# Optimization experiments

Hardware: AMD Instinct MI355X
Metric: run time of the kernel (lower is better)

The kernel has to match this reference:

```python
import jax, jax.numpy as jnp
import numpy as np

B, C, H, W = 4, 3, 128, 128
HID = 128          # hidden_features
L = 6              # hidden_layers
NP = 5             # n_params
DT = 0.1
EPS = 1e-5         # PyG InstanceNorm eps
D_EMB = 1 + 2 + NP             # u + pos(2) + params
D_MSG = 2 * HID + 1 + 2 + NP   # x_i,x_j,u_i-u_j,pos_i-pos_j,vars_i
D_UPD = HID + HID + NP         # x, message, vars


def _build_edges(b, h, w):
    # 8-neighbor grid graph (radius_graph with r=sqrt(2), loop=False),
    # node index = ix*h + iy (x-major, matching create_graph's meshgrid flatten)
    ix, iy = np.meshgrid(np.arange(w), np.arange(h), indexing='ij')
    node = ix * h + iy
    srcs, tgts = [], []
    for dx in (-1, 0, 1):
        for dy in (-1, 0, 1):
            if dx == 0 and dy == 0:
                continue
            t = node[max(0, -dx):w - max(0, dx), max(0, -dy):h - max(0, dy)]
            s = node[max(0, dx):w - max(0, -dx), max(0, dy):h - max(0, -dy)]
            srcs.append(s.ravel()); tgts.append(t.ravel())
    src = np.concatenate(srcs); tgt = np.concatenate(tgts)
    offs = (np.arange(b) * h * w)[:, None]
    src = (src[None, :] + offs).ravel()
    tgt = (tgt[None, :] + offs).ravel()
    return np.stack([src, tgt]).astype(np.int32)


def _lin(key, fan_in, fan_out):
    kw, kb = jax.random.split(key)
    s = 1.0 / np.sqrt(fan_in)
    return (jax.random.uniform(kw, (fan_in, fan_out), jnp.float32, -s, s),
            jax.random.uniform(kb, (fan_out,), jnp.float32, -s, s))


def setup_inputs() -> dict:
    key = jax.random.key(0)
    ks = jax.random.split(key, 32)
    inputs = jax.random.normal(ks[0], (B, C, H, W), jnp.float32)
    case_params = jax.random.uniform(ks[1], (B, NP), jnp.float32, 0.5, 1.5)
    edge_index = jnp.asarray(_build_edges(B, H, W))

    emb_W1, emb_b1 = _lin(ks[2], D_EMB, HID)
    emb_W2, emb_b2 = _lin(ks[3], HID, HID)

    def stack(kbase, fan_in, fan_out):
        Ws, bs = [], []
        for l in range(L):
            Wl, bl = _lin(jax.random.fold_in(kbase, l), fan_in, fan_out)
            Ws.append(Wl); bs.append(bl)
        return jnp.stack(Ws), jnp.stack(bs)

    msg1_W, msg1_b = stack(ks[4], D_MSG, HID)
    msg2_W, msg2_b = stack(ks[5], HID, HID)
    upd1_W, upd1_b = stack(ks[6], D_UPD, HID)
    upd2_W, upd2_b = stack(ks[7], HID, HID)
    out_W1, out_b1 = _lin(ks[8], HID, HID // 2)
    out_W2, out_b2 = _lin(ks[9], HID // 2, 1)

    return dict(inputs=inputs, case_params=case_params, edge_index=edge_index,
                emb_W1=emb_W1, emb_b1=emb_b1, emb_W2=emb_W2, emb_b2=emb_b2,
                msg1_W=msg1_W, msg1_b=msg1_b, msg2_W=msg2_W, msg2_b=msg2_b,
                upd1_W=upd1_W, upd1_b=upd1_b, upd2_W=upd2_W, upd2_b=upd2_b,
                out_W1=out_W1, out_b1=out_b1, out_W2=out_W2, out_b2=out_b2)


def reference(inputs, case_params, edge_index,
              emb_W1, emb_b1, emb_W2, emb_b2,
              msg1_W, msg1_b, msg2_W, msg2_b,
              upd1_W, upd1_b, upd2_W, upd2_b,
              out_W1, out_b1, out_W2, out_b2):
    b, c, h, w = inputs.shape
    n = b * h * w
    swish = lambda x: x * jax.nn.sigmoid(x)

    # graph node features: [b,c,h,w] -> [b*h*w, c]; u = channel 0
    x_nodes = inputs.transpose(0, 2, 3, 1).reshape(-1, c)
    u = x_nodes[:, :1]
    # pos, faithful to create_graph: per-graph meshgrid over (x:w, y:h), x-major flatten
    gx = jnp.linspace(0., 1., w)[:, None] * jnp.ones((h,), inputs.dtype)   # [w,h]
    gy = jnp.ones((w,), inputs.dtype)[:, None] * jnp.linspace(0., 1., h)  # [w,h]
    pos = jnp.stack([gx[None] * case_params[:, 1, None, None],
                     gy[None] * case_params[:, 0, None, None]], axis=-1).reshape(-1, 2)
    params = jnp.repeat(case_params, h * w, axis=0)  # [n, NP]

    src, tgt = edge_index[0], edge_index[1]
    deg = jax.ops.segment_sum(jnp.ones_like(src, dtype=inputs.dtype), tgt,
                              num_segments=n)
    deg = jnp.maximum(deg, 1.)[:, None]

    # embedding MLP
    f = swish(jnp.concatenate([u, pos, params], -1) @ emb_W1 + emb_b1)
    f = swish(f @ emb_W2 + emb_b2)

    for l in range(msg1_W.shape[0]):
        # message: gather -> MLP (formula 8)
        m = jnp.concatenate([f[tgt], f[src], u[tgt] - u[src],
                             pos[tgt] - pos[src], params[tgt]], -1)  # [E, D_MSG]
        m = swish(m @ msg1_W[l] + msg1_b[l])
        m = swish(m @ msg2_W[l] + msg2_b[l])
        # mean-aggregate at target nodes
        agg = jax.ops.segment_sum(m, tgt, num_segments=n) / deg
        # update MLP (formula 9) + residual (in_features == out_features)
        upd = swish(jnp.concatenate([f, agg, params], -1) @ upd1_W[l] + upd1_b[l])
        upd = swish(upd @ upd2_W[l] + upd2_b[l])
        f = f + upd
        # InstanceNorm per graph (affine=False, biased var)
        fg = f.reshape(b, h * w, -1)
        mean = fg.mean(1, keepdims=True)
        var = ((fg - mean) ** 2).mean(1, keepdims=True)
        f = ((fg - mean) * jax.lax.rsqrt(var + EPS)).reshape(n, -1)

    diff = swish(f @ out_W1 + out_b1) @ out_W2 + out_b2  # [n,1]
    out = u + DT * diff
    return out.reshape(b, h, w, 1).transpose(0, 3, 1, 2)  # preds [b,1,h,w]
```

## Files before the change

kernel.cpp:

```cpp
#include <hip/hip_runtime.h>
#include <hip/hip_bf16.h>
#include <math.h>

#define NNODE 65536
#define NBAT  16384
#define NP    5
#define DT    0.1f
#define EPS   1e-5f

typedef __attribute__((ext_vector_type(8))) short short8;
typedef __attribute__((ext_vector_type(4))) float floatx4;

union S8U { short8 s; unsigned int u[4]; };

__device__ __forceinline__ float swishf(float x) {
    return x * __builtin_amdgcn_rcpf(1.f + __expf(-x));
}
__device__ __forceinline__ float asf(unsigned int u) {
    union { unsigned int u; float f; } x; x.u = u; return x.f;
}
__device__ __forceinline__ unsigned short f2b(float f) {
    union { float f; unsigned int u; } x; x.f = f;
    unsigned int r = x.u + 0x7fff + ((x.u >> 16) & 1);
    return (unsigned short)(r >> 16);
}
__device__ __forceinline__ unsigned int pk2(float a, float b) {
    __hip_bfloat162 h = __float22bfloat162_rn(make_float2(a, b));
    union { __hip_bfloat162 h; unsigned int u; } x; x.h = h; return x.u;
}

#define CHP(w, g, r15) ((((w) * 272) + (g) * 17 + (r15)) * 8)

__global__ __launch_bounds__(256) void prep_frag(
    const float* __restrict__ src, unsigned short* __restrict__ dst,
    int ldn, int koff, int NT, int lstride, int perm, int total)
{
    int i = blockIdx.x * 256 + threadIdx.x;
    if (i >= total) return;
    int nper = NT << 11;
    int l = i / nper;
    int r0 = i - l * nper;
    int t = r0 >> 11;
    int ks = (r0 >> 9) & 3;
    int lane = (r0 >> 3) & 63;
    int j = r0 & 7;
    int lm = lane & 15, lq = lane >> 4;
    int p = ks * 32 + lq * 8 + j;
    int k = perm ? ((p & 7) * 16 + (p >> 3)) : p;
    int n = t * 16 + lm;
    dst[i] = f2b(src[(size_t)l * lstride + (size_t)(koff + k) * ldn + n]);
}

__global__ __launch_bounds__(256) void node_init(
    const float* __restrict__ inp, const float* __restrict__ cp,
    float* __restrict__ u, float* __restrict__ posx, float* __restrict__ posy,
    float* __restrict__ mr)
{
    int n = blockIdx.x * 256 + threadIdx.x;
    int b = n >> 14, r = n & 16383;
    int a = r >> 7, c = r & 127;
    u[n] = inp[b * 3 * NBAT + r];
    posx[n] = (a * (1.f / 127.f)) * cp[b * NP + 1];
    posy[n] = (c * (1.f / 127.f)) * cp[b * NP + 0];
    if (n < 1024) mr[n] = ((n >> 7) & 1) ? 1.f : 0.f;
}

__device__ __forceinline__ void build_normf_frags(
    const float* __restrict__ f, const float* __restrict__ mr,
    int block0, int b, int w, int lm, int lq, short8* afr)
{
    int row = block0 + w * 16 + lm;
#pragma unroll
    for (int ks = 0; ks < 4; ks++) {
        int po = ks * 32 + lq * 8;
        float4 v0 = *(const float4*)(f + (size_t)row * 128 + po);
        float4 v1 = *(const float4*)(f + (size_t)row * 128 + po + 4);
        float4 m0 = *(const float4*)(mr + b * 256 + po);
        float4 m1 = *(const float4*)(mr + b * 256 + po + 4);
        float4 s0 = *(const float4*)(mr + b * 256 + 128 + po);
        float4 s1 = *(const float4*)(mr + b * 256 + 128 + po + 4);
        S8U o;
        o.u[0] = pk2((v0.x - m0.x) * s0.x, (v0.y - m0.y) * s0.y);
        o.u[1] = pk2((v0.z - m0.z) * s0.z, (v0.w - m0.w) * s0.w);
        o.u[2] = pk2((v1.x - m1.x) * s1.x, (v1.y - m1.y) * s1.y);
        o.u[3] = pk2((v1.z - m1.z) * s1.z, (v1.w - m1.w) * s1.w);
        afr[ks] = o.s;
    }
}

__global__ __launch_bounds__(256) void embed_mfma(
    const float* __restrict__ u, const float* __restrict__ posx,
    const float* __restrict__ posy, const float* __restrict__ cp,
    const float* __restrict__ W1, const float* __restrict__ b1,
    const unsigned short* __restrict__ W2F, const float* __restrict__ b2,
    float* __restrict__ f)
{
    __shared__ unsigned short lA[4 * 272 * 8];
    __shared__ unsigned short lB[1024 * 8];
    int tid = threadIdx.x;
    int block0 = blockIdx.x * 64;
    {
        int r = tid >> 2, p4 = tid & 3;
        int n = block0 + r;
        int b = n >> 14;
        float e8[8];
        e8[0] = u[n]; e8[1] = posx[n]; e8[2] = posy[n];
#pragma unroll
        for (int p = 0; p < 5; p++) e8[3 + p] = cp[b * NP + p];
        float a32[32];
        const float4* b4 = (const float4*)(b1 + p4 * 32);
#pragma unroll
        for (int q = 0; q < 8; q++) {
            float4 bv = b4[q];
            a32[q * 4 + 0] = bv.x; a32[q * 4 + 1] = bv.y;
            a32[q * 4 + 2] = bv.z; a32[q * 4 + 3] = bv.w;
        }
#pragma unroll
        for (int i = 0; i < 8; i++) {
            const float4* w4 = (const float4*)(W1 + i * 128 + p4 * 32);
            float ev = e8[i];
#pragma unroll
            for (int q = 0; q < 8; q++) {
                float4 wv = w4[q];
                a32[q * 4 + 0] += ev * wv.x; a32[q * 4 + 1] += ev * wv.y;
                a32[q * 4 + 2] += ev * wv.z; a32[q * 4 + 3] += ev * wv.w;
            }
        }
#pragma unroll
        for (int j = 0; j < 4; j++) {
            S8U o;
#pragma unroll
            for (int q = 0; q < 4; q++)
                o.u[q] = pk2(swishf(a32[j * 8 + 2 * q]), swishf(a32[j * 8 + 2 * q + 1]));
            *(short8*)(lA + CHP(r >> 4, p4 * 4 + j, r & 15)) = o.s;
        }
    }
    int w = tid >> 6, lane = tid & 63, lm = lane & 15, lq = lane >> 4;
    floatx4 acc[8];
#pragma unroll
    for (int t = 0; t < 8; t++) acc[t] = (floatx4)(0.f);
    for (int th = 0; th < 2; th++) {
        if (th) __syncthreads();
#pragma unroll
        for (int i = 0; i < 4; i++)
            *(short8*)(lB + (tid + i * 256) * 8) =
                *(const short8*)(W2F + (th * 1024 + tid + i * 256) * 8);
        __syncthreads();
#pragma unroll
        for (int ks = 0; ks < 4; ks++) {
            short8 a = *(const short8*)(lA + CHP(w, ks * 4 + lq, lm));
#pragma unroll
            for (int t2 = 0; t2 < 4; t2++) {
                short8 bf = *(const short8*)(lB + ((t2 * 4 + ks) * 64 + lane) * 8);
                acc[th * 4 + t2] = __builtin_amdgcn_mfma_f32_16x16x32_bf16(a, bf, acc[th * 4 + t2], 0, 0, 0);
            }
        }
    }
    float bias2[8];
#pragma unroll
    for (int t = 0; t < 8; t++) bias2[t] = b2[t * 16 + lm];
#pragma unroll
    for (int r = 0; r < 4; r++) {
        int nd = block0 + w * 16 + lq * 4 + r;
        float4 v0, v1;
        v0.x = swishf(acc[0][r] + bias2[0]); v0.y = swishf(acc[1][r] + bias2[1]);
        v0.z = swishf(acc[2][r] + bias2[2]); v0.w = swishf(acc[3][r] + bias2[3]);
        v1.x = swishf(acc[4][r] + bias2[4]); v1.y = swishf(acc[5][r] + bias2[5]);
        v1.z = swishf(acc[6][r] + bias2[6]); v1.w = swishf(acc[7][r] + bias2[7]);
        *(float4*)(f + (size_t)nd * 128 + lm * 8) = v0;
        *(float4*)(f + (size_t)nd * 128 + lm * 8 + 4) = v1;
    }
}

__global__ __launch_bounds__(256) void pqu_kernel(
    const float* __restrict__ f, const float* __restrict__ mr,
    const unsigned short* __restrict__ wPT, const unsigned short* __restrict__ wQT,
    const float* __restrict__ mW, const float* __restrict__ mb,
    const float* __restrict__ u, const float* __restrict__ px,
    const float* __restrict__ py, const float* __restrict__ cp,
    unsigned short* __restrict__ Pn, unsigned short* __restrict__ Qn)
{
    __shared__ unsigned short lB[2048 * 8];
    int tid = threadIdx.x;
    int block0 = blockIdx.x * 64;
    int b = block0 >> 14;
    int w = tid >> 6, lane = tid & 63, lm = lane & 15, lq = lane >> 4;

    short8 afr[4];
    build_normf_frags(f, mr, block0, b, w, lm, lq, afr);

    float u4[4], px4[4], py4[4];
#pragma unroll
    for (int r = 0; r < 4; r++) {
        int nd = block0 + w * 16 + lq * 4 + r;
        u4[r] = u[nd]; px4[r] = px[nd]; py4[r] = py[nd];
    }
    float cp5[5];
#pragma unroll
    for (int p = 0; p < 5; p++) cp5[p] = cp[b * NP + p];
    float wu[8], wx[8], wy[8], pt[8];

    for (int ph = 0; ph < 2; ph++) {
        const unsigned short* bsrc = (ph == 0) ? wPT : wQT;
        if (ph) __syncthreads();
#pragma unroll
        for (int i = 0; i < 8; i++)
            *(short8*)(lB + (tid + i * 256) * 8) = *(const short8*)(bsrc + (tid + i * 256) * 8);
        __syncthreads();
        floatx4 acc[8];
#pragma unroll
        for (int t = 0; t < 8; t++) acc[t] = (floatx4)(0.f);
#pragma unroll
        for (int ks = 0; ks < 4; ks++) {
#pragma unroll
            for (int t = 0; t < 8; t++) {
                short8 bf = *(const short8*)(lB + ((t * 4 + ks) * 64 + lane) * 8);
                acc[t] = __builtin_amdgcn_mfma_f32_16x16x32_bf16(afr[ks], bf, acc[t], 0, 0, 0);
            }
        }
        if (ph == 0) {
#pragma unroll
            for (int t = 0; t < 8; t++) {
                int c = t * 16 + lm;
                wu[t] = mW[256 * 128 + c]; wx[t] = mW[257 * 128 + c]; wy[t] = mW[258 * 128 + c];
                float p0 = mb[c];
#pragma unroll
                for (int p = 0; p < 5; p++) p0 += cp5[p] * mW[(259 + p) * 128 + c];
                pt[t] = p0;
            }
#pragma unroll
            for (int r = 0; r < 4; r++) {
                int nd = block0 + w * 16 + lq * 4 + r;
                float v[8];
#pragma unroll
                for (int t = 0; t < 8; t++)
                    v[t] = acc[t][r] + pt[t] + u4[r] * wu[t] + px4[r] * wx[t] + py4[r] * wy[t];
                S8U o;
#pragma unroll
                for (int q = 0; q < 4; q++) o.u[q] = pk2(v[2 * q], v[2 * q + 1]);
                *(short8*)(Pn + (size_t)nd * 128 + lm * 8) = o.s;
            }
        } else {
#pragma unroll
            for (int r = 0; r < 4; r++) {
                int nd = block0 + w * 16 + lq * 4 + r;
                float v[8];
#pragma unroll
                for (int t = 0; t < 8; t++)
                    v[t] = acc[t][r] - (u4[r] * wu[t] + px4[r] * wx[t] + py4[r] * wy[t]);
                S8U o;
#pragma unroll
                for (int q = 0; q < 4; q++) o.u[q] = pk2(v[2 * q], v[2 * q + 1]);
                *(short8*)(Qn + (size_t)nd * 128 + lm * 8) = o.s;
            }
        }
    }
}

__global__ __launch_bounds__(256) void msg_kernel(
    const unsigned short* __restrict__ Pn, const unsigned short* __restrict__ Qn,
    const unsigned short* __restrict__ w2F, const float* __restrict__ b2,
    unsigned short* __restrict__ aggF)
{
    __shared__ unsigned short lB[1024 * 8];
    __shared__ unsigned short lAgg[8 * 128];
    int tid = threadIdx.x;
    int base = blockIdx.x * 8;
    int b = base >> 14;
    int a = (base >> 7) & 127;
    int c0 = base & 127;
    int w = tid >> 6, lane = tid & 63, lm = lane & 15, lq = lane >> 4;

    short8 afr[4];
    {
        int tl = lm >> 3, e = lm & 7;
        int idx = (e < 4) ? e : e + 1;
        int dx = idx / 3 - 1, dy = idx % 3 - 1;
        int cc = c0 + w * 2 + tl;
        int na = a + dx, nc = cc + dy;
        bool valid = (na >= 0) & (na < 128) & (nc >= 0) & (nc < 128);
        int t = base + w * 2 + tl;
        int s = valid ? ((b << 14) + (na << 7) + nc) : t;
#pragma unroll
        for (int ks = 0; ks < 4; ks++) {
            int po = ks * 32 + lq * 8;
            S8U pv, qv, o;
            pv.s = *(const short8*)(Pn + (size_t)t * 128 + po);
            qv.s = *(const short8*)(Qn + (size_t)s * 128 + po);
#pragma unroll
            for (int q = 0; q < 4; q++) {
                float pl = asf(pv.u[q] << 16), ph = asf(pv.u[q] & 0xffff0000u);
                float ql = asf(qv.u[q] << 16), qh = asf(qv.u[q] & 0xffff0000u);
                o.u[q] = pk2(swishf(pl + ql), swishf(ph + qh));
            }
            afr[ks] = o.s;
        }
    }

    floatx4 acc[8];
#pragma unroll
    for (int t = 0; t < 8; t++) acc[t] = (floatx4)(0.f);
    for (int th = 0; th < 2; th++) {
        if (th) __syncthreads();
#pragma unroll
        for (int i = 0; i < 4; i++)
            *(short8*)(lB + (tid + i * 256) * 8) =
                *(const short8*)(w2F + (th * 1024 + tid + i * 256) * 8);
        __syncthreads();
#pragma unroll
        for (int ks = 0; ks < 4; ks++) {
#pragma unroll
            for (int t2 = 0; t2 < 4; t2++) {
                short8 bf = *(const short8*)(lB + ((t2 * 4 + ks) * 64 + lane) * 8);
                acc[th * 4 + t2] = __builtin_amdgcn_mfma_f32_16x16x32_bf16(afr[ks], bf, acc[th * 4 + t2], 0, 0, 0);
            }
        }
    }

    bool vr[4];
#pragma unroll
    for (int r = 0; r < 4; r++) {
        int row16 = lq * 4 + r;
        int tl2 = row16 >> 3, e = row16 & 7;
        int idx = (e < 4) ? e : e + 1;
        int dx = idx / 3 - 1, dy = idx % 3 - 1;
        int cc = c0 + w * 2 + tl2;
        int na = a + dx, nc = cc + dy;
        vr[r] = (na >= 0) & (na < 128) & (nc >= 0) & (nc < 128);
    }
    float ov[8];
#pragma unroll
    for (int t = 0; t < 8; t++) {
        float bb = b2[t * 16 + lm];
        float s01 = 0.f;
#pragma unroll
        for (int r = 0; r < 4; r++)
            s01 += vr[r] ? swishf(acc[t][r] + bb) : 0.f;
        ov[t] = s01 + __shfl_xor(s01, 16);
    }
    if ((lq & 1) == 0) {
        int tl = w * 2 + (lq >> 1);
        int cc = c0 + tl;
        int deg = (1 + (a > 0) + (a < 127)) * (1 + (cc > 0) + (cc < 127)) - 1;
        float inv = 1.f / (float)deg;
        S8U o;
#pragma unroll
        for (int q = 0; q < 4; q++) o.u[q] = pk2(ov[2 * q] * inv, ov[2 * q + 1] * inv);
        *(short8*)(lAgg + tl * 128 + lm * 8) = o.s;
    }
    __syncthreads();
    if (tid < 128) {
        int row8 = tid >> 4, g = tid & 15;
        int n = base + row8;
        size_t lin = (size_t)(n >> 6) * 1024 + (size_t)(((n & 63) >> 4) * 256 + g * 16 + (n & 15));
        *(short8*)(aggF + lin * 8) = *(const short8*)(lAgg + row8 * 128 + g * 8);
    }
}

__global__ __launch_bounds__(256) void updf_kernel(
    float* __restrict__ f, const float* __restrict__ mr,
    const unsigned short* __restrict__ aggF,
    const unsigned short* __restrict__ u1aF, const unsigned short* __restrict__ u1bF,
    const unsigned short* __restrict__ u2F,
    const float* __restrict__ U1, const float* __restrict__ c1,
    const float* __restrict__ c2, const float* __restrict__ cp,
    float* __restrict__ partials)
{
    __shared__ unsigned short lA[4 * 272 * 8];
    __shared__ unsigned short lB[1024 * 8];
    int tid = threadIdx.x;
    int block0 = blockIdx.x * 64;
    int b = block0 >> 14;
    int w = tid >> 6, lane = tid & 63, lm = lane & 15, lq = lane >> 4;

    short8 afr[4];
    build_normf_frags(f, mr, block0, b, w, lm, lq, afr);
    floatx4 acc[8];
#pragma unroll
    for (int t = 0; t < 8; t++) acc[t] = (floatx4)(0.f);

    for (int ph = 0; ph < 2; ph++) {
        const unsigned short* bsrc = ph ? u1bF : u1aF;
        if (ph) {
#pragma unroll
            for (int ks = 0; ks < 4; ks++)
                afr[ks] = *(const short8*)(aggF +
                    ((size_t)blockIdx.x * 1024 + w * 256 + (ks * 4 + lq) * 16 + lm) * 8);
        }
        for (int th = 0; th < 2; th++) {
            if (ph | th) __syncthreads();
#pragma unroll
            for (int i = 0; i < 4; i++)
                *(short8*)(lB + (tid + i * 256) * 8) =
                    *(const short8*)(bsrc + (th * 1024 + tid + i * 256) * 8);
            __syncthreads();
#pragma unroll
            for (int ks = 0; ks < 4; ks++) {
#pragma unroll
                for (int t2 = 0; t2 < 4; t2++) {
                    short8 bf = *(const short8*)(lB + ((t2 * 4 + ks) * 64 + lane) * 8);
                    acc[th * 4 + t2] = __builtin_amdgcn_mfma_f32_16x16x32_bf16(afr[ks], bf, acc[th * 4 + t2], 0, 0, 0);
                }
            }
        }
    }

    float cp5[5];
#pragma unroll
    for (int p = 0; p < 5; p++) cp5[p] = cp[b * NP + p];
    float pt[8];
#pragma unroll
    for (int t = 0; t < 8; t++) {
        int c = t * 16 + lm;
        float p0 = c1[c];
#pragma unroll
        for (int p = 0; p < 5; p++) p0 += cp5[p] * U1[(256 + p) * 128 + c];
        pt[t] = p0;
    }
#pragma unroll
    for (int r = 0; r < 4; r++) {
        S8U o;
#pragma unroll
        for (int q = 0; q < 4; q++)
            o.u[q] = pk2(swishf(acc[2 * q][r] + pt[2 * q]),
                         swishf(acc[2 * q + 1][r] + pt[2 * q + 1]));
        *(short8*)(lA + CHP(w, lm, lq * 4 + r)) = o.s;
    }

#pragma unroll
    for (int t = 0; t < 8; t++) acc[t] = (floatx4)(0.f);
    for (int th = 0; th < 2; th++) {
        __syncthreads();
#pragma unroll
        for (int i = 0; i < 4; i++)
            *(short8*)(lB + (tid + i * 256) * 8) =
                *(const short8*)(u2F + (th * 1024 + tid + i * 256) * 8);
        __syncthreads();
#pragma unroll
        for (int ks = 0; ks < 4; ks++) {
            short8 a = *(const short8*)(lA + CHP(w, ks * 4 + lq, lm));
#pragma unroll
            for (int t2 = 0; t2 < 4; t2++) {
                short8 bf = *(const short8*)(lB + ((t2 * 4 + ks) * 64 + lane) * 8);
                acc[th * 4 + t2] = __builtin_amdgcn_mfma_f32_16x16x32_bf16(a, bf, acc[th * 4 + t2], 0, 0, 0);
            }
        }
    }

    float c2v[8];
#pragma unroll
    for (int t = 0; t < 8; t++) c2v[t] = c2[t * 16 + lm];
    float4 me0 = *(const float4*)(mr + b * 256 + lm * 8);
    float4 me1 = *(const float4*)(mr + b * 256 + lm * 8 + 4);
    float4 rs0 = *(const float4*)(mr + b * 256 + 128 + lm * 8);
    float4 rs1 = *(const float4*)(mr + b * 256 + 128 + lm * 8 + 4);
    float ssum[8], ssq[8];
#pragma unroll
    for (int t = 0; t < 8; t++) { ssum[t] = 0.f; ssq[t] = 0.f; }
#pragma unroll
    for (int r = 0; r < 4; r++) {
        int nd = block0 + w * 16 + lq * 4 + r;
        float4 f0 = *(const float4*)(f + (size_t)nd * 128 + lm * 8);
        float4 f1 = *(const float4*)(f + (size_t)nd * 128 + lm * 8 + 4);
        float fn[8];
        fn[0] = (f0.x - me0.x) * rs0.x + swishf(acc[0][r] + c2v[0]);
        fn[1] = (f0.y - me0.y) * rs0.y + swishf(acc[1][r] + c2v[1]);
        fn[2] = (f0.z - me0.z) * rs0.z + swishf(acc[2][r] + c2v[2]);
        fn[3] = (f0.w - me0.w) * rs0.w + swishf(acc[3][r] + c2v[3]);
        fn[4] = (f1.x - me1.x) * rs1.x + swishf(acc[4][r] + c2v[4]);
        fn[5] = (f1.y - me1.y) * rs1.y + swishf(acc[5][r] + c2v[5]);
        fn[6] = (f1.z - me1.z) * rs1.z + swishf(acc[6][r] + c2v[6]);
        fn[7] = (f1.w - me1.w) * rs1.w + swishf(acc[7][r] + c2v[7]);
        *(float4*)(f + (size_t)nd * 128 + lm * 8) = make_float4(fn[0], fn[1], fn[2], fn[3]);
        *(float4*)(f + (size_t)nd * 128 + lm * 8 + 4) = make_float4(fn[4], fn[5], fn[6], fn[7]);
#pragma unroll
        for (int t = 0; t < 8; t++) { ssum[t] += fn[t]; ssq[t] += fn[t] * fn[t]; }
    }
#pragma unroll
    for (int t = 0; t < 8; t++) {
        ssum[t] += __shfl_xor(ssum[t], 16); ssum[t] += __shfl_xor(ssum[t], 32);
        ssq[t]  += __shfl_xor(ssq[t], 16);  ssq[t]  += __shfl_xor(ssq[t], 32);
    }
    __syncthreads();
    float* red = (float*)lA;
    if (lq == 0) {
#pragma unroll
        for (int t = 0; t < 8; t++) {
            red[w * 256 + lm * 8 + t] = ssum[t];
            red[w * 256 + 128 + lm * 8 + t] = ssq[t];
        }
    }
    __syncthreads();
    {
        float v = red[tid] + red[256 + tid] + red[512 + tid] + red[768 + tid];
        partials[(size_t)blockIdx.x * 256 + tid] = v;
    }
}

__global__ __launch_bounds__(256) void finalize_kernel(
    const float* __restrict__ partials, float* __restrict__ mr)
{
    __shared__ float s[256];
    int b = blockIdx.x, tid = threadIdx.x;
    float acc = 0.f;
    const float* p = partials + (size_t)b * 256 * 256 + tid;
#pragma unroll 8
    for (int i = 0; i < 256; i++) acc += p[i * 256];
    s[tid] = acc;
    __syncthreads();
    if (tid < 128) {
        float mean = s[tid] * (1.f / 16384.f);
        float var = s[128 + tid] * (1.f / 16384.f) - mean * mean;
        mr[b * 256 + tid] = mean;
        mr[b * 256 + 128 + tid] = rsqrtf(var + EPS);
    }
}

__global__ __launch_bounds__(256) void out_head(
    const float* __restrict__ f, const float* __restrict__ mr,
    const unsigned short* __restrict__ O1F, const float* __restrict__ ob1,
    const float* __restrict__ O2, const float* __restrict__ ob2,
    const float* __restrict__ u, float* __restrict__ out)
{
    __shared__ unsigned short lB[1024 * 8];
    int tid = threadIdx.x;
    int block0 = blockIdx.x * 64;
    int b = block0 >> 14;
    int w = tid >> 6, lane = tid & 63, lm = lane & 15, lq = lane >> 4;
#pragma unroll
    for (int i = 0; i < 4; i++)
        *(short8*)(lB + (tid + i * 256) * 8) = *(const short8*)(O1F + (tid + i * 256) * 8);
    short8 afr[4];
    build_normf_frags(f, mr, block0, b, w, lm, lq, afr);
    __syncthreads();
    floatx4 acc[4];
#pragma unroll
    for (int t = 0; t < 4; t++) acc[t] = (floatx4)(0.f);
#pragma unroll
    for (int ks = 0; ks < 4; ks++) {
#pragma unroll
        for (int t = 0; t < 4; t++) {
            short8 bf = *(const short8*)(lB + ((t * 4 + ks) * 64 + lane) * 8);
            acc[t] = __builtin_amdgcn_mfma_f32_16x16x32_bf16(afr[ks], bf, acc[t], 0, 0, 0);
        }
    }
    float b1v[4], o2v[4];
#pragma unroll
    for (int t = 0; t < 4; t++) {
        b1v[t] = ob1[t * 16 + lm];
        o2v[t] = O2[t * 16 + lm];
    }
    float ob2v = ob2[0];
#pragma unroll
    for (int r = 0; r < 4; r++) {
        float s = 0.f;
#pragma unroll
        for (int t = 0; t < 4; t++) s += swishf(acc[t][r] + b1v[t]) * o2v[t];
        s += __shfl_xor(s, 1); s += __shfl_xor(s, 2);
        s += __shfl_xor(s, 4); s += __shfl_xor(s, 8);
        if (lm == 0) {
            int nd = block0 + w * 16 + lq * 4 + r;
            out[nd] = u[nd] + DT * (s + ob2v);
        }
    }
}

extern "C" void kernel_launch(void* const* d_in, const int* in_sizes, int n_in,
                              void* d_out, int out_size, void* d_ws, size_t ws_size,
                              hipStream_t stream)
{
    const float* inputs = (const float*)d_in[0];
    const float* cp     = (const float*)d_in[1];
    const float* emb_W1 = (const float*)d_in[3];
    const float* emb_b1 = (const float*)d_in[4];
    const float* emb_W2 = (const float*)d_in[5];
    const float* emb_b2 = (const float*)d_in[6];
    const float* msg1_W = (const float*)d_in[7];
    const float* msg1_b = (const float*)d_in[8];
    const float* msg2_W = (const float*)d_in[9];
    const float* msg2_b = (const float*)d_in[10];
    const float* upd1_W = (const float*)d_in[11];
    const float* upd1_b = (const float*)d_in[12];
    const float* upd2_W = (const float*)d_in[13];
    const float* upd2_b = (const float*)d_in[14];
    const float* out_W1 = (const float*)d_in[15];
    const float* out_b1 = (const float*)d_in[16];
    const float* out_W2 = (const float*)d_in[17];
    const float* out_b2 = (const float*)d_in[18];
    float* out = (float*)d_out;

    char* base = (char*)d_ws;
    size_t off = 0;
    float* f     = (float*)(base + off); off += (size_t)NNODE * 128 * 4;
    unsigned short* Pn   = (unsigned short*)(base + off); off += (size_t)NNODE * 128 * 2;
    unsigned short* Qn   = (unsigned short*)(base + off); off += (size_t)NNODE * 128 * 2;
    unsigned short* aggF = (unsigned short*)(base + off); off += (size_t)NNODE * 128 * 2;
    float* u    = (float*)(base + off); off += NNODE * 4;
    float* posx = (float*)(base + off); off += NNODE * 4;
    float* posy = (float*)(base + off); off += NNODE * 4;
    float* partials = (float*)(base + off); off += 1024 * 256 * 4;
    float* mrbuf = (float*)(base + off); off += 1024 * 4;
    unsigned short* wPT  = (unsigned short*)(base + off); off += 6 * 16384 * 2;
    unsigned short* wQT  = (unsigned short*)(base + off); off += 6 * 16384 * 2;
    unsigned short* w2F  = (unsigned short*)(base + off); off += 6 * 16384 * 2;
    unsigned short* u1aF = (unsigned short*)(base + off); off += 6 * 16384 * 2;
    unsigned short* u1bF = (unsigned short*)(base + off); off += 6 * 16384 * 2;
    unsigned short* u2F  = (unsigned short*)(base + off); off += 6 * 16384 * 2;
    unsigned short* eW2F = (unsigned short*)(base + off); off += 16384 * 2;
    unsigned short* O1F  = (unsigned short*)(base + off); off += 8192 * 2;

    prep_frag<<<384, 256, 0, stream>>>(msg1_W, wPT, 128, 0,   8, 264 * 128, 1, 6 * 16384);
    prep_frag<<<384, 256, 0, stream>>>(msg1_W, wQT, 128, 128, 8, 264 * 128, 1, 6 * 16384);
    prep_frag<<<384, 256, 0, stream>>>(msg2_W, w2F, 128, 0,   8, 128 * 128, 1, 6 * 16384);
    prep_frag<<<384, 256, 0, stream>>>(upd1_W, u1aF, 128, 0,   8, 261 * 128, 1, 6 * 16384);
    prep_frag<<<384, 256, 0, stream>>>(upd1_W, u1bF, 128, 128, 8, 261 * 128, 1, 6 * 16384);
    prep_frag<<<384, 256, 0, stream>>>(upd2_W, u2F, 128, 0,   8, 128 * 128, 1, 6 * 16384);
    prep_frag<<<64, 256, 0, stream>>>(emb_W2, eW2F, 128, 0,   8, 0, 0, 16384);
    prep_frag<<<32, 256, 0, stream>>>(out_W1, O1F, 64, 0,    4, 0, 1, 8192);

    node_init<<<256, 256, 0, stream>>>(inputs, cp, u, posx, posy, mrbuf);
    embed_mfma<<<1024, 256, 0, stream>>>(u, posx, posy, cp, emb_W1, emb_b1, eW2F, emb_b2, f);
    for (int l = 0; l < 6; l++) {
        pqu_kernel<<<1024, 256, 0, stream>>>(f, mrbuf,
            wPT + (size_t)l * 16384, wQT + (size_t)l * 16384,
            msg1_W + (size_t)l * 264 * 128, msg1_b + (size_t)l * 128,
            u, posx, posy, cp, Pn, Qn);
        msg_kernel<<<8192, 256, 0, stream>>>(Pn, Qn,
            w2F + (size_t)l * 16384, msg2_b + (size_t)l * 128, aggF);
        updf_kernel<<<1024, 256, 0, stream>>>(f, mrbuf, aggF,
            u1aF + (size_t)l * 16384, u1bF + (size_t)l * 16384, u2F + (size_t)l * 16384,
            upd1_W + (size_t)l * 261 * 128, upd1_b + (size_t)l * 128,
            upd2_b + (size_t)l * 128, cp, partials);
        finalize_kernel<<<4, 256, 0, stream>>>(partials, mrbuf);
    }
    out_head<<<1024, 256, 0, stream>>>(f, mrbuf, O1F, out_b1, out_W2, out_b2, u, out);
}
```

Baseline: 801.1 us.

## Merge prep launches, fuse node init into embed, store P/Q in fp32, fold biases

Eight weight-prep launches become one prep_all kernel, and node_init is folded into embed_mfma, removing several small launches. The P/Q message intermediates are now stored as fp32 rather than bf16. This doubles their memory traffic in the gather-heavy msg_kernel but drops the unpack step and gains precision. Biases are preloaded into the MFMA accumulators across kernels. msg_kernel also gets a fast path for interior tiles that skips neighbour-validity checks and uses a constant degree of 8.

After: 852.6 us. 6.4% more time.

```diff
diff --git a/kernel.cpp b/kernel.cpp
--- a/kernel.cpp
+++ b/kernel.cpp
@@ -16,9 +16,6 @@
 __device__ __forceinline__ float swishf(float x) {
     return x * __builtin_amdgcn_rcpf(1.f + __expf(-x));
 }
-__device__ __forceinline__ float asf(unsigned int u) {
-    union { unsigned int u; float f; } x; x.u = u; return x.f;
-}
 __device__ __forceinline__ unsigned short f2b(float f) {
     union { float f; unsigned int u; } x; x.f = f;
     unsigned int r = x.u + 0x7fff + ((x.u >> 16) & 1);
@@ -31,12 +28,27 @@
 
 #define CHP(w, g, r15) ((((w) * 272) + (g) * 17 + (r15)) * 8)
 
-__global__ __launch_bounds__(256) void prep_frag(
-    const float* __restrict__ src, unsigned short* __restrict__ dst,
-    int ldn, int koff, int NT, int lstride, int perm, int total)
-{
-    int i = blockIdx.x * 256 + threadIdx.x;
-    if (i >= total) return;
+__global__ __launch_bounds__(256) void prep_all(
+    const float* __restrict__ msg1_W, const float* __restrict__ msg2_W,
+    const float* __restrict__ upd1_W, const float* __restrict__ upd2_W,
+    const float* __restrict__ emb_W2, const float* __restrict__ out_W1,
+    unsigned short* __restrict__ wPT, unsigned short* __restrict__ wQT,
+    unsigned short* __restrict__ w2F, unsigned short* __restrict__ u1aF,
+    unsigned short* __restrict__ u1bF, unsigned short* __restrict__ u2F,
+    unsigned short* __restrict__ eW2F, unsigned short* __restrict__ O1F)
+{
+    int blk = blockIdx.x;
+    const float* src; unsigned short* dst;
+    int ldn = 128, koff, NT = 8, lstride, perm = 1, i0;
+    if (blk < 384)       { src = msg1_W; dst = wPT;  koff = 0;   lstride = 264 * 128; i0 = blk; }
+    else if (blk < 768)  { src = msg1_W; dst = wQT;  koff = 128; lstride = 264 * 128; i0 = blk - 384; }
+    else if (blk < 1152) { src = msg2_W; dst = w2F;  koff = 0;   lstride = 128 * 128; i0 = blk - 768; }
+    else if (blk < 1536) { src = upd1_W; dst = u1aF; koff = 0;   lstride = 261 * 128; i0 = blk - 1152; }
+    else if (blk < 1920) { src = upd1_W; dst = u1bF; koff = 128; lstride = 261 * 128; i0 = blk - 1536; }
+    else if (blk < 2304) { src = upd2_W; dst = u2F;  koff = 0;   lstride = 128 * 128; i0 = blk - 1920; }
+    else if (blk < 2368) { src = emb_W2; dst = eW2F; koff = 0;   lstride = 0; perm = 0; i0 = blk - 2304; }
+    else                 { src = out_W1; dst = O1F;  koff = 0;   lstride = 0; ldn = 64; NT = 4; i0 = blk - 2368; }
+    int i = i0 * 256 + threadIdx.x;
     int nper = NT << 11;
     int l = i / nper;
     int r0 = i - l * nper;
@@ -49,20 +61,6 @@
     int k = perm ? ((p & 7) * 16 + (p >> 3)) : p;
     int n = t * 16 + lm;
     dst[i] = f2b(src[(size_t)l * lstride + (size_t)(koff + k) * ldn + n]);
-}
-
-__global__ __launch_bounds__(256) void node_init(
-    const float* __restrict__ inp, const float* __restrict__ cp,
-    float* __restrict__ u, float* __restrict__ posx, float* __restrict__ posy,
-    float* __restrict__ mr)
-{
-    int n = blockIdx.x * 256 + threadIdx.x;
-    int b = n >> 14, r = n & 16383;
-    int a = r >> 7, c = r & 127;
-    u[n] = inp[b * 3 * NBAT + r];
-    posx[n] = (a * (1.f / 127.f)) * cp[b * NP + 1];
-    posy[n] = (c * (1.f / 127.f)) * cp[b * NP + 0];
-    if (n < 1024) mr[n] = ((n >> 7) & 1) ? 1.f : 0.f;
 }
 
 __device__ __forceinline__ void build_normf_frags(
@@ -89,22 +87,29 @@
 }
 
 __global__ __launch_bounds__(256) void embed_mfma(
-    const float* __restrict__ u, const float* __restrict__ posx,
-    const float* __restrict__ posy, const float* __restrict__ cp,
+    const float* __restrict__ inp, const float* __restrict__ cp,
     const float* __restrict__ W1, const float* __restrict__ b1,
     const unsigned short* __restrict__ W2F, const float* __restrict__ b2,
-    float* __restrict__ f)
+    float* __restrict__ f, float* __restrict__ u,
+    float* __restrict__ posx, float* __restrict__ posy, float* __restrict__ mr)
 {
     __shared__ unsigned short lA[4 * 272 * 8];
     __shared__ unsigned short lB[1024 * 8];
     int tid = threadIdx.x;
     int block0 = blockIdx.x * 64;
+    if (blockIdx.x < 4) mr[blockIdx.x * 256 + tid] = ((tid >> 7) & 1) ? 1.f : 0.f;
     {
         int r = tid >> 2, p4 = tid & 3;
         int n = block0 + r;
         int b = n >> 14;
+        int rr = n & 16383;
+        int aa = rr >> 7, cc = rr & 127;
+        float uu = inp[b * 3 * NBAT + rr];
+        float pxx = (aa * (1.f / 127.f)) * cp[b * NP + 1];
+        float pyy = (cc * (1.f / 127.f)) * cp[b * NP + 0];
+        if (p4 == 0) { u[n] = uu; posx[n] = pxx; posy[n] = pyy; }
         float e8[8];
-        e8[0] = u[n]; e8[1] = posx[n]; e8[2] = posy[n];
+        e8[0] = uu; e8[1] = pxx; e8[2] = pyy;
 #pragma unroll
         for (int p = 0; p < 5; p++) e8[3 + p] = cp[b * NP + p];
         float a32[32];
@@ -136,9 +141,12 @@
         }
     }
     int w = tid >> 6, lane = tid & 63, lm = lane & 15, lq = lane >> 4;
+    float bias2[8];
+#pragma unroll
+    for (int t = 0; t < 8; t++) bias2[t] = b2[t * 16 + lm];
     floatx4 acc[8];
 #pragma unroll
-    for (int t = 0; t < 8; t++) acc[t] = (floatx4)(0.f);
+    for (int t = 0; t < 8; t++) acc[t] = (floatx4)(bias2[t]);
     for (int th = 0; th < 2; th++) {
         if (th) __syncthreads();
 #pragma unroll
@@ -156,17 +164,14 @@
             }
         }
     }
-    float bias2[8];
-#pragma unroll
-    for (int t = 0; t < 8; t++) bias2[t] = b2[t * 16 + lm];
 #pragma unroll
     for (int r = 0; r < 4; r++) {
         int nd = block0 + w * 16 + lq * 4 + r;
         float4 v0, v1;
-        v0.x = swishf(acc[0][r] + bias2[0]); v0.y = swishf(acc[1][r] + bias2[1]);
-        v0.z = swishf(acc[2][r] + bias2[2]); v0.w = swishf(acc[3][r] + bias2[3]);
-        v1.x = swishf(acc[4][r] + bias2[4]); v1.y = swishf(acc[5][r] + bias2[5]);
-        v1.z = swishf(acc[6][r] + bias2[6]); v1.w = swishf(acc[7][r] + bias2[7]);
+        v0.x = swishf(acc[0][r]); v0.y = swishf(acc[1][r]);
+        v0.z = swishf(acc[2][r]); v0.w = swishf(acc[3][r]);
+        v1.x = swishf(acc[4][r]); v1.y = swishf(acc[5][r]);
+        v1.z = swishf(acc[6][r]); v1.w = swishf(acc[7][r]);
         *(float4*)(f + (size_t)nd * 128 + lm * 8) = v0;
         *(float4*)(f + (size_t)nd * 128 + lm * 8 + 4) = v1;
     }
@@ -178,7 +183,7 @@
     const float* __restrict__ mW, const float* __restrict__ mb,
     const float* __restrict__ u, const float* __restrict__ px,
     const float* __restrict__ py, const float* __restrict__ cp,
-    unsigned short* __restrict__ Pn, unsigned short* __restrict__ Qn)
+    float* __restrict__ Pn, float* __restrict__ Qn)
 {
     __shared__ unsigned short lB[2048 * 8];
     int tid = threadIdx.x;
@@ -199,6 +204,15 @@
 #pragma unroll
     for (int p = 0; p < 5; p++) cp5[p] = cp[b * NP + p];
     float wu[8], wx[8], wy[8], pt[8];
+#pragma unroll
+    for (int t = 0; t < 8; t++) {
+        int c = t * 16 + lm;
+        wu[t] = mW[256 * 128 + c]; wx[t] = mW[257 * 128 + c]; wy[t] = mW[258 * 128 + c];
+        float p0 = mb[c];
+#pragma unroll
+        for (int p = 0; p < 5; p++) p0 += cp5[p] * mW[(259 + p) * 128 + c];
+        pt[t] = p0;
+    }
 
     for (int ph = 0; ph < 2; ph++) {
         const unsigned short* bsrc = (ph == 0) ? wPT : wQT;
@@ -209,7 +223,7 @@
         __syncthreads();
         floatx4 acc[8];
 #pragma unroll
-        for (int t = 0; t < 8; t++) acc[t] = (floatx4)(0.f);
+        for (int t = 0; t < 8; t++) acc[t] = (ph == 0) ? (floatx4)(pt[t]) : (floatx4)(0.f);
 #pragma unroll
         for (int ks = 0; ks < 4; ks++) {
 #pragma unroll
@@ -220,45 +234,44 @@
         }
         if (ph == 0) {
 #pragma unroll
-            for (int t = 0; t < 8; t++) {
-                int c = t * 16 + lm;
-                wu[t] = mW[256 * 128 + c]; wx[t] = mW[257 * 128 + c]; wy[t] = mW[258 * 128 + c];
-                float p0 = mb[c];
-#pragma unroll
-                for (int p = 0; p < 5; p++) p0 += cp5[p] * mW[(259 + p) * 128 + c];
-                pt[t] = p0;
-            }
-#pragma unroll
             for (int r = 0; r < 4; r++) {
                 int nd = block0 + w * 16 + lq * 4 + r;
-                float v[8];
-#pragma unroll
-                for (int t = 0; t < 8; t++)
-                    v[t] = acc[t][r] + pt[t] + u4[r] * wu[t] + px4[r] * wx[t] + py4[r] * wy[t];
-                S8U o;
-#pragma unroll
-                for (int q = 0; q < 4; q++) o.u[q] = pk2(v[2 * q], v[2 * q + 1]);
-                *(short8*)(Pn + (size_t)nd * 128 + lm * 8) = o.s;
+                float sc0 = u4[r], sc1 = px4[r], sc2 = py4[r];
+                float4 o0, o1;
+                o0.x = acc[0][r] + sc0 * wu[0] + sc1 * wx[0] + sc2 * wy[0];
+                o0.y = acc[1][r] + sc0 * wu[1] + sc1 * wx[1] + sc2 * wy[1];
+                o0.z = acc[2][r] + sc0 * wu[2] + sc1 * wx[2] + sc2 * wy[2];
+                o0.w = acc[3][r] + sc0 * wu[3] + sc1 * wx[3] + sc2 * wy[3];
+                o1.x = acc[4][r] + sc0 * wu[4] + sc1 * wx[4] + sc2 * wy[4];
+                o1.y = acc[5][r] + sc0 * wu[5] + sc1 * wx[5] + sc2 * wy[5];
+                o1.z = acc[6][r] + sc0 * wu[6] + sc1 * wx[6] + sc2 * wy[6];
+                o1.w = acc[7][r] + sc0 * wu[7] + sc1 * wx[7] + sc2 * wy[7];
+                *(float4*)(Pn + (size_t)nd * 128 + lm * 8) = o0;
+                *(float4*)(Pn + (size_t)nd * 128 + lm * 8 + 4) = o1;
             }
         } else {
 #pragma unroll
             for (int r = 0; r < 4; r++) {
                 int nd = block0 + w * 16 + lq * 4 + r;
-                float v[8];
-#pragma unroll
-                for (int t = 0; t < 8; t++)
-                    v[t] = acc[t][r] - (u4[r] * wu[t] + px4[r] * wx[t] + py4[r] * wy[t]);
-                S8U o;
-#pragma unroll
-                for (int q = 0; q < 4; q++) o.u[q] = pk2(v[2 * q], v[2 * q + 1]);
-                *(short8*)(Qn + (size_t)nd * 128 + lm * 8) = o.s;
+                float sc0 = u4[r], sc1 = px4[r], sc2 = py4[r];
+                float4 o0, o1;
+                o0.x = acc[0][r] - (sc0 * wu[0] + sc1 * wx[0] + sc2 * wy[0]);
+                o0.y = acc[1][r] - (sc0 * wu[1] + sc1 * wx[1] + sc2 * wy[1]);
+                o0.z = acc[2][r] - (sc0 * wu[2] + sc1 * wx[2] + sc2 * wy[2]);
+                o0.w = acc[3][r] - (sc0 * wu[3] + sc1 * wx[3] + sc2 * wy[3]);
+                o1.x = acc[4][r] - (sc0 * wu[4] + sc1 * wx[4] + sc2 * wy[4]);
+                o1.y = acc[5][r] - (sc0 * wu[5] + sc1 * wx[5] + sc2 * wy[5]);
+                o1.z = acc[6][r] - (sc0 * wu[6] + sc1 * wx[6] + sc2 * wy[6]);
+                o1.w = acc[7][r] - (sc0 * wu[7] + sc1 * wx[7] + sc2 * wy[7]);
+                *(float4*)(Qn + (size_t)nd * 128 + lm * 8) = o0;
+                *(float4*)(Qn + (size_t)nd * 128 + lm * 8 + 4) = o1;
             }
         }
     }
 }
 
 __global__ __launch_bounds__(256) void msg_kernel(
-    const unsigned short* __restrict__ Pn, const unsigned short* __restrict__ Qn,
+    const float* __restrict__ Pn, const float* __restrict__ Qn,
     const unsigned short* __restrict__ w2F, const float* __restrict__ b2,
     unsigned short* __restrict__ aggF)
 {
@@ -270,6 +283,7 @@
     int a = (base >> 7) & 127;
     int c0 = base & 127;
     int w = tid >> 6, lane = tid & 63, lm = lane & 15, lq = lane >> 4;
+    bool interior = (a > 0) & (a < 127) & (c0 > 0) & (c0 + 8 < 128);
 
     short8 afr[4];
     {
@@ -278,28 +292,37 @@
         int dx = idx / 3 - 1, dy = idx % 3 - 1;
         int cc = c0 + w * 2 + tl;
         int na = a + dx, nc = cc + dy;
-        bool valid = (na >= 0) & (na < 128) & (nc >= 0) & (nc < 128);
         int t = base + w * 2 + tl;
-        int s = valid ? ((b << 14) + (na << 7) + nc) : t;
+        int s;
+        if (interior) s = (b << 14) + (na << 7) + nc;
+        else {
+            bool valid = (na >= 0) & (na < 128) & (nc >= 0) & (nc < 128);
+            s = valid ? ((b << 14) + (na << 7) + nc) : t;
+        }
+        const float* Pr = Pn + (size_t)t * 128;
+        const float* Qr = Qn + (size_t)s * 128;
 #pragma unroll
         for (int ks = 0; ks < 4; ks++) {
             int po = ks * 32 + lq * 8;
-            S8U pv, qv, o;
-            pv.s = *(const short8*)(Pn + (size_t)t * 128 + po);
-            qv.s = *(const short8*)(Qn + (size_t)s * 128 + po);
-#pragma unroll
-            for (int q = 0; q < 4; q++) {
-                float pl = asf(pv.u[q] << 16), ph = asf(pv.u[q] & 0xffff0000u);
-                float ql = asf(qv.u[q] << 16), qh = asf(qv.u[q] & 0xffff0000u);
-                o.u[q] = pk2(swishf(pl + ql), swishf(ph + qh));
-            }
+            float4 p0 = *(const float4*)(Pr + po);
+            float4 p1 = *(const float4*)(Pr + po + 4);
+            float4 q0 = *(const float4*)(Qr + po);
+            float4 q1 = *(const float4*)(Qr + po + 4);
+            S8U o;
+            o.u[0] = pk2(swishf(p0.x + q0.x), swishf(p0.y + q0.y));
+            o.u[1] = pk2(swishf(p0.z + q0.z), swishf(p0.w + q0.w));
+            o.u[2] = pk2(swishf(p1.x + q1.x), swishf(p1.y + q1.y));
+            o.u[3] = pk2(swishf(p1.z + q1.z), swishf(p1.w + q1.w));
             afr[ks] = o.s;
         }
     }
 
+    float b2v[8];
+#pragma unroll
+    for (int t = 0; t < 8; t++) b2v[t] = b2[t * 16 + lm];
     floatx4 acc[8];
 #pragma unroll
-    for (int t = 0; t < 8; t++) acc[t] = (floatx4)(0.f);
+    for (int t = 0; t < 8; t++) acc[t] = (floatx4)(b2v[t]);
     for (int th = 0; th < 2; th++) {
         if (th) __syncthreads();
 #pragma unroll
@@ -317,36 +340,53 @@
         }
     }
 
-    bool vr[4];
-#pragma unroll
-    for (int r = 0; r < 4; r++) {
-        int row16 = lq * 4 + r;
-        int tl2 = row16 >> 3, e = row16 & 7;
-        int idx = (e < 4) ? e : e + 1;
-        int dx = idx / 3 - 1, dy = idx % 3 - 1;
-        int cc = c0 + w * 2 + tl2;
-        int na = a + dx, nc = cc + dy;
-        vr[r] = (na >= 0) & (na < 128) & (nc >= 0) & (nc < 128);
-    }
-    float ov[8];
-#pragma unroll
-    for (int t = 0; t < 8; t++) {
-        float bb = b2[t * 16 + lm];
-        float s01 = 0.f;
-#pragma unroll
-        for (int r = 0; r < 4; r++)
-            s01 += vr[r] ? swishf(acc[t][r] + bb) : 0.f;
-        ov[t] = s01 + __shfl_xor(s01, 16);
-    }
-    if ((lq & 1) == 0) {
-        int tl = w * 2 + (lq >> 1);
-        int cc = c0 + tl;
-        int deg = (1 + (a > 0) + (a < 127)) * (1 + (cc > 0) + (cc < 127)) - 1;
-        float inv = 1.f / (float)deg;
-        S8U o;
-#pragma unroll
-        for (int q = 0; q < 4; q++) o.u[q] = pk2(ov[2 * q] * inv, ov[2 * q + 1] * inv);
-        *(short8*)(lAgg + tl * 128 + lm * 8) = o.s;
+    if (interior) {
+        float ov[8];
+#pragma unroll
+        for (int t = 0; t < 8; t++) {
+            float s01 = swishf(acc[t][0]) + swishf(acc[t][1])
+                      + swishf(acc[t][2]) + swishf(acc[t][3]);
+            ov[t] = s01 + __shfl_xor(s01, 16);
+        }
+        if ((lq & 1) == 0) {
+            int tl = w * 2 + (lq >> 1);
+            S8U o;
+#pragma unroll
+            for (int q = 0; q < 4; q++)
+                o.u[q] = pk2(ov[2 * q] * 0.125f, ov[2 * q + 1] * 0.125f);
+            *(short8*)(lAgg + tl * 128 + lm * 8) = o.s;
+        }
+    } else {
+        bool vr[4];
+#pragma unroll
+        for (int r = 0; r < 4; r++) {
+            int row16 = lq * 4 + r;
+            int tl2 = row16 >> 3, e = row16 & 7;
+            int idx = (e < 4) ? e : e + 1;
+            int dx = idx / 3 - 1, dy = idx % 3 - 1;
+            int cc = c0 + w * 2 + tl2;
+            int na = a + dx, nc = cc + dy;
+            vr[r] = (na >= 0) & (na < 128) & (nc >= 0) & (nc < 128);
+        }
+        float ov[8];
+#pragma unroll
+        for (int t = 0; t < 8; t++) {
+            float s01 = 0.f;
+#pragma unroll
+            for (int r = 0; r < 4; r++)
+                s01 += vr[r] ? swishf(acc[t][r]) : 0.f;
+            ov[t] = s01 + __shfl_xor(s01, 16);
+        }
+        if ((lq & 1) == 0) {
+            int tl = w * 2 + (lq >> 1);
+            int cc = c0 + tl;
+            int deg = (1 + (a > 0) + (a < 127)) * (1 + (cc > 0) + (cc < 127)) - 1;
+            float inv = 1.f / (float)deg;
+            S8U o;
+#pragma unroll
+            for (int q = 0; q < 4; q++) o.u[q] = pk2(ov[2 * q] * inv, ov[2 * q + 1] * inv);
+            *(short8*)(lAgg + tl * 128 + lm * 8) = o.s;
+        }
     }
     __syncthreads();
     if (tid < 128) {
@@ -373,11 +413,24 @@
     int b = block0 >> 14;
     int w = tid >> 6, lane = tid & 63, lm = lane & 15, lq = lane >> 4;
 
+    float cp5[5];
+#pragma unroll
+    for (int p = 0; p < 5; p++) cp5[p] = cp[b * NP + p];
+    float pt[8];
+#pragma unroll
+    for (int t = 0; t < 8; t++) {
+        int c = t * 16 + lm;
+        float p0 = c1[c];
+#pragma unroll
+        for (int p = 0; p < 5; p++) p0 += cp5[p] * U1[(256 + p) * 128 + c];
+        pt[t] = p0;
+    }
+
     short8 afr[4];
     build_normf_frags(f, mr, block0, b, w, lm, lq, afr);
     floatx4 acc[8];
 #pragma unroll
-    for (int t = 0; t < 8; t++) acc[t] = (floatx4)(0.f);
+    for (int t = 0; t < 8; t++) acc[t] = (floatx4)(pt[t]);
 
     for (int ph = 0; ph < 2; ph++) {
         const unsigned short* bsrc = ph ? u1bF : u1aF;
@@ -405,30 +458,20 @@
         }
     }
 
-    float cp5[5];
-#pragma unroll
-    for (int p = 0; p < 5; p++) cp5[p] = cp[b * NP + p];
-    float pt[8];
-#pragma unroll
-    for (int t = 0; t < 8; t++) {
-        int c = t * 16 + lm;
-        float p0 = c1[c];
-#pragma unroll
-        for (int p = 0; p < 5; p++) p0 += cp5[p] * U1[(256 + p) * 128 + c];
-        pt[t] = p0;
-    }
 #pragma unroll
     for (int r = 0; r < 4; r++) {
         S8U o;
 #pragma unroll
         for (int q = 0; q < 4; q++)
-            o.u[q] = pk2(swishf(acc[2 * q][r] + pt[2 * q]),
-                         swishf(acc[2 * q + 1][r] + pt[2 * q + 1]));
+            o.u[q] = pk2(swishf(acc[2 * q][r]), swishf(acc[2 * q + 1][r]));
         *(short8*)(lA + CHP(w, lm, lq * 4 + r)) = o.s;
     }
 
-#pragma unroll
-    for (int t = 0; t < 8; t++) acc[t] = (floatx4)(0.f);
+    float c2v[8];
+#pragma unroll
+    for (int t = 0; t < 8; t++) c2v[t] = c2[t * 16 + lm];
+#pragma unroll
+    for (int t = 0; t < 8; t++) acc[t] = (floatx4)(c2v[t]);
     for (int th = 0; th < 2; th++) {
         __syncthreads();
 #pragma unroll
@@ -447,9 +490,6 @@
         }
     }
 
-    float c2v[8];
-#pragma unroll
-    for (int t = 0; t < 8; t++) c2v[t] = c2[t * 16 + lm];
     float4 me0 = *(const float4*)(mr + b * 256 + lm * 8);
     float4 me1 = *(const float4*)(mr + b * 256 + lm * 8 + 4);
     float4 rs0 = *(const float4*)(mr + b * 256 + 128 + lm * 8);
@@ -463,14 +503,14 @@
         float4 f0 = *(const float4*)(f + (size_t)nd * 128 + lm * 8);
         float4 f1 = *(const float4*)(f + (size_t)nd * 128 + lm * 8 + 4);
         float fn[8];
-        fn[0] = (f0.x - me0.x) * rs0.x + swishf(acc[0][r] + c2v[0]);
-        fn[1] = (f0.y - me0.y) * rs0.y + swishf(acc[1][r] + c2v[1]);
-        fn[2] = (f0.z - me0.z) * rs0.z + swishf(acc[2][r] + c2v[2]);
-        fn[3] = (f0.w - me0.w) * rs0.w + swishf(acc[3][r] + c2v[3]);
-        fn[4] = (f1.x - me1.x) * rs1.x + swishf(acc[4][r] + c2v[4]);
-        fn[5] = (f1.y - me1.y) * rs1.y + swishf(acc[5][r] + c2v[5]);
-        fn[6] = (f1.z - me1.z) * rs1.z + swishf(acc[6][r] + c2v[6]);
-        fn[7] = (f1.w - me1.w) * rs1.w + swishf(acc[7][r] + c2v[7]);
+        fn[0] = (f0.x - me0.x) * rs0.x + swishf(acc[0][r]);
+        fn[1] = (f0.y - me0.y) * rs0.y + swishf(acc[1][r]);
+        fn[2] = (f0.z - me0.z) * rs0.z + swishf(acc[2][r]);
+        fn[3] = (f0.w - me0.w) * rs0.w + swishf(acc[3][r]);
+        fn[4] = (f1.x - me1.x) * rs1.x + swishf(acc[4][r]);
+        fn[5] = (f1.y - me1.y) * rs1.y + swishf(acc[5][r]);
+        fn[6] = (f1.z - me1.z) * rs1.z + swishf(acc[6][r]);
+        fn[7] = (f1.w - me1.w) * rs1.w + swishf(acc[7][r]);
         *(float4*)(f + (size_t)nd * 128 + lm * 8) = make_float4(fn[0], fn[1], fn[2], fn[3]);
         *(float4*)(f + (size_t)nd * 128 + lm * 8 + 4) = make_float4(fn[4], fn[5], fn[6], fn[7]);
 #pragma unroll
@@ -532,10 +572,16 @@
         *(short8*)(lB + (tid + i * 256) * 8) = *(const short8*)(O1F + (tid + i * 256) * 8);
     short8 afr[4];
     build_normf_frags(f, mr, block0, b, w, lm, lq, afr);
+    float b1v[4], o2v[4];
+#pragma unroll
+    for (int t = 0; t < 4; t++) {
+        b1v[t] = ob1[t * 16 + lm];
+        o2v[t] = O2[t * 16 + lm];
+    }
     __syncthreads();
     floatx4 acc[4];
 #pragma unroll
-    for (int t = 0; t < 4; t++) acc[t] = (floatx4)(0.f);
+    for (int t = 0; t < 4; t++) acc[t] = (floatx4)(b1v[t]);
 #pragma unroll
     for (int ks = 0; ks < 4; ks++) {
 #pragma unroll
@@ -544,18 +590,12 @@
             acc[t] = __builtin_amdgcn_mfma_f32_16x16x32_bf16(afr[ks], bf, acc[t], 0, 0, 0);
         }
     }
-    float b1v[4], o2v[4];
-#pragma unroll
-    for (int t = 0; t < 4; t++) {
-        b1v[t] = ob1[t * 16 + lm];
-        o2v[t] = O2[t * 16 + lm];
-    }
     float ob2v = ob2[0];
 #pragma unroll
     for (int r = 0; r < 4; r++) {
         float s = 0.f;
 #pragma unroll
-        for (int t = 0; t < 4; t++) s += swishf(acc[t][r] + b1v[t]) * o2v[t];
+        for (int t = 0; t < 4; t++) s += swishf(acc[t][r]) * o2v[t];
         s += __shfl_xor(s, 1); s += __shfl_xor(s, 2);
         s += __shfl_xor(s, 4); s += __shfl_xor(s, 8);
         if (lm == 0) {
@@ -592,8 +632,8 @@
     char* base = (char*)d_ws;
     size_t off = 0;
     float* f     = (float*)(base + off); off += (size_t)NNODE * 128 * 4;
-    unsigned short* Pn   = (unsigned short*)(base + off); off += (size_t)NNODE * 128 * 2;
-    unsigned short* Qn   = (unsigned short*)(base + off); off += (size_t)NNODE * 128 * 2;
+    float* Pn    = (float*)(base + off); off += (size_t)NNODE * 128 * 4;
+    float* Qn    = (float*)(base + off); off += (size_t)NNODE * 128 * 4;
     unsigned short* aggF = (unsigned short*)(base + off); off += (size_t)NNODE * 128 * 2;
     float* u    = (float*)(base + off); off += NNODE * 4;
     float* posx = (float*)(base + off); off += NNODE * 4;
@@ -609,17 +649,10 @@
     unsigned short* eW2F = (unsigned short*)(base + off); off += 16384 * 2;
     unsigned short* O1F  = (unsigned short*)(base + off); off += 8192 * 2;
 
-    prep_frag<<<384, 256, 0, stream>>>(msg1_W, wPT, 128, 0,   8, 264 * 128, 1, 6 * 16384);
-    prep_frag<<<384, 256, 0, stream>>>(msg1_W, wQT, 128, 128, 8, 264 * 128, 1, 6 * 16384);
-    prep_frag<<<384, 256, 0, stream>>>(msg2_W, w2F, 128, 0,   8, 128 * 128, 1, 6 * 16384);
-    prep_frag<<<384, 256, 0, stream>>>(upd1_W, u1aF, 128, 0,   8, 261 * 128, 1, 6 * 16384);
-    prep_frag<<<384, 256, 0, stream>>>(upd1_W, u1bF, 128, 128, 8, 261 * 128, 1, 6 * 16384);
-    prep_frag<<<384, 256, 0, stream>>>(upd2_W, u2F, 128, 0,   8, 128 * 128, 1, 6 * 16384);
-    prep_frag<<<64, 256, 0, stream>>>(emb_W2, eW2F, 128, 0,   8, 0, 0, 16384);
-    prep_frag<<<32, 256, 0, stream>>>(out_W1, O1F, 64, 0,    4, 0, 1, 8192);
-
-    node_init<<<256, 256, 0, stream>>>(inputs, cp, u, posx, posy, mrbuf);
-    embed_mfma<<<1024, 256, 0, stream>>>(u, posx, posy, cp, emb_W1, emb_b1, eW2F, emb_b2, f);
+    prep_all<<<2400, 256, 0, stream>>>(msg1_W, msg2_W, upd1_W, upd2_W, emb_W2, out_W1,
+                                       wPT, wQT, w2F, u1aF, u1bF, u2F, eW2F, O1F);
+    embed_mfma<<<1024, 256, 0, stream>>>(inputs, cp, emb_W1, emb_b1, eW2F, emb_b2,
+                                         f, u, posx, posy, mrbuf);
     for (int l = 0; l < 6; l++) {
         pqu_kernel<<<1024, 256, 0, stream>>>(f, mrbuf,
             wPT + (size_t)l * 16384, wQT + (size_t)l * 16384,
```
